# Kernel tuning notes

Hardware: AMD Instinct MI355X
Metric: run time of the kernel (lower is better)

## Reference

```python
import jax, jax.numpy as jnp
import numpy as np
import math

N = 512  # num particles
D = 128  # particle dimension


def setup_inputs() -> dict:
    key = jax.random.key(0)
    particles = jax.random.normal(key, (N, D), dtype=jnp.float32)
    return {"particles": particles}


def reference(particles):
    # particles: [N, D]
    n = particles.shape[0]
    # delta_x[i, j] = particles[j] - particles[i]  (matches unsqueeze(0) - unsqueeze(1))
    delta_x = particles[None, :, :] - particles[:, None, :]   # [N, N, D]
    norm_sq = delta_x * delta_x                               # [N, N, D]

    # mode='univ': per-dimension median over strictly-upper-triangular pairs
    iu_r, iu_c = np.triu_indices(n, k=1)                      # static indices
    sel = norm_sq[iu_r, iu_c, :]                              # [M, D], M = N(N-1)/2
    m = sel.shape[0]
    # torch.median returns the LOWER of the two middle values for even counts
    median = jnp.sort(sel, axis=0)[(m - 1) // 2]              # [D]

    h = median / math.log(n + 1)
    bandwidth = jnp.maximum(h, jnp.asarray(1e-9, dtype=h.dtype))  # [D]

    log_kernel = -(norm_sq / bandwidth)                       # [N, N, D]
    grad_log_kernel = -2.0 * delta_x / bandwidth              # [N, N, D]
    return log_kernel, grad_log_kernel
```

## Files before the change

### kernel.cpp

```cpp
#include <hip/hip_runtime.h>
#include <hip/hip_bf16.h>

#define NP 512
#define DD 128
#define NPAIRS (NP * (NP - 1) / 2)

__device__ __forceinline__ float bitonic512(float r, int tid, float* lds)
{
    for (int k = 2; k <= NP; k <<= 1) {
        for (int s = k >> 1; s > 0; s >>= 1) {
            float other;
            if (s < 64) {
                other = __shfl_xor(r, s);
            } else {
                __syncthreads();
                lds[tid] = r;
                __syncthreads();
                other = lds[tid ^ s];
            }
            const bool lower = (tid & s) == 0;
            const bool up    = (tid & k) == 0;
            r = (lower == up) ? fminf(r, other) : fmaxf(r, other);
        }
    }
    return r;
}

__global__ void __launch_bounds__(512)
median_bw_kernel(const float* __restrict__ particles, float* __restrict__ inv_bw)
{
    const int d = blockIdx.x, tid = threadIdx.x, lane = tid & 63, wid = tid >> 6;

    __shared__ float v[NP];
    __shared__ float cand[NP];
    __shared__ int   cnt_s[2][8];
    __shared__ float sum_s[8];
    __shared__ int   scan_s[8];

    float r = particles[tid * DD + d];
    r = bitonic512(r, tid, v);
    __syncthreads();
    v[tid] = r;
    __syncthreads();

    const float vj = r;
    const int want1 = (NPAIRS - 1) / 2 + 1;

    float s = (tid >= 150) ? (vj - v[tid - 150]) : 0.0f;
    #pragma unroll
    for (int off = 32; off > 0; off >>= 1) s += __shfl_xor(s, off);
    if (lane == 0) sum_s[wid] = s;
    __syncthreads();
    float msum = 0.0f;
    #pragma unroll
    for (int w = 0; w < 8; ++w) msum += sum_s[w];
    const float meanp = fmaxf(msum / 362.0f, 0.0f);

    const float maxd = v[NP - 1] - v[0];
    unsigned lo = 0u;
    unsigned hi = __float_as_uint(maxd) + 1u;
    int C_lo = 0;
    int C_hi = NPAIRS;
    int A = 0, B = tid;
    int buf = 0, round = 0;

    float g_lo = 0.5f - (float)want1;
    float g_hi = (float)(NPAIRS - want1) + 0.5f;
    int   last = 0;

    while (lo < hi) {
        if (C_hi - C_lo <= NP) break;

        const unsigned span = hi - lo;
        unsigned mid;
        if (round == 0) {
            mid = __float_as_uint(meanp);
        } else if ((round & 3) == 3) {
            mid = lo + (span >> 1);
        } else {
            const float flo = __uint_as_float(lo);
            const float fhi = __uint_as_float(hi);
            const float xn  = (flo * g_hi - fhi * g_lo) / (g_hi - g_lo);
            mid = __float_as_uint(xn);
        }
        const unsigned dlt = span >> 3;
        if (mid < lo + dlt)            mid = lo + dlt;
        if (mid > hi - 1u - dlt)       mid = (hi - 1u) - dlt;
        if (mid < lo)                  mid = lo;
        if (mid > hi - 1u)             mid = hi - 1u;
        const float x = __uint_as_float(mid);

        int a = A, b = B;
        while (a < b) {
            const int   m  = (a + b) >> 1;
            const float pv = v[m];
            const bool  t  = (vj - pv <= x);
            b = t ? m : b;
            a = t ? a : m + 1;
        }
        int cnt = tid - a;

        #pragma unroll
        for (int off = 32; off > 0; off >>= 1) cnt += __shfl_xor(cnt, off);
        if (lane == 0) cnt_s[buf][wid] = cnt;
        __syncthreads();
        int tot = 0;
        #pragma unroll
        for (int w = 0; w < 8; ++w) tot += cnt_s[buf][w];

        if (tot >= want1) {
            hi = mid; C_hi = tot; A = a;
            g_hi = (float)(tot - want1) + 0.5f;
            if (last == 1) g_lo *= 0.5f;
            last = 1;
        } else {
            lo = mid + 1u; C_lo = tot; B = a;
            g_lo = (float)(tot - want1) + 0.5f;
            if (last == -1) g_hi *= 0.5f;
            last = -1;
        }
        buf ^= 1;
        ++round;
    }

    if (lo >= hi) {
        if (tid == 0) {
            const float Dk = __uint_as_float(lo);
            const float h  = (Dk * Dk) / 6.240275844172107f;
            inv_bw[d] = 1.0f / fmaxf(h, 1e-9f);
        }
    } else {
        const int T  = C_hi - C_lo;
        const int rr = min(want1 - C_lo, T);
        const int n  = B - A;
        int inc = n;
        #pragma unroll
        for (int off = 1; off < 64; off <<= 1) {
            const int t = __shfl_up(inc, off);
            if (lane >= off) inc += t;
        }
        if (lane == 63) scan_s[wid] = inc;
        __syncthreads();
        int woff = 0;
        #pragma unroll
        for (int w = 0; w < 8; ++w) woff += (w < wid) ? scan_s[w] : 0;
        int off0 = woff + inc - n;
        for (int i = A; i < B; ++i) cand[off0++] = vj - v[i];
        __syncthreads();

        float c = (tid < T) ? cand[tid] : INFINITY;
        c = bitonic512(c, tid, v);

        if (tid == rr - 1) {
            const float Dk = c;
            const float h  = (Dk * Dk) / 6.240275844172107f;
            inv_bw[d] = 1.0f / fmaxf(h, 1e-9f);
        }
    }
}

__global__ void __launch_bounds__(256)
stein_out_kernel(const float* __restrict__ particles,
                 const float* __restrict__ inv_bw,
                 float4* __restrict__ out_lk,
                 float4* __restrict__ out_g)
{
    const float4* __restrict__ p4  = (const float4*)particles;
    const float4* __restrict__ ib4 = (const float4*)inv_bw;
    const int total = NP * NP * (DD / 4);

    for (int t = blockIdx.x * blockDim.x + threadIdx.x; t < total;
         t += gridDim.x * blockDim.x) {
        const int d4 = t & (DD / 4 - 1);
        const int j  = (t >> 5) & (NP - 1);
        const int i  = t >> 14;

        const float4 xj = p4[j * (DD / 4) + d4];
        const float4 xi = p4[i * (DD / 4) + d4];
        const float4 ib = ib4[d4];

        float4 lk, g;
        {
            const float dx = xj.x - xi.x;
            lk.x = -(dx * dx * ib.x);
            g.x  = -2.0f * dx * ib.x;
        }
        {
            const float dx = xj.y - xi.y;
            lk.y = -(dx * dx * ib.y);
            g.y  = -2.0f * dx * ib.y;
        }
        {
            const float dx = xj.z - xi.z;
            lk.z = -(dx * dx * ib.z);
            g.z  = -2.0f * dx * ib.z;
        }
        {
            const float dx = xj.w - xi.w;
            lk.w = -(dx * dx * ib.w);
            g.w  = -2.0f * dx * ib.w;
        }
        out_lk[t] = lk;
        out_g[t]  = g;
    }
}

extern "C" void kernel_launch(void* const* d_in, const int* in_sizes, int n_in,
                              void* d_out, int out_size, void* d_ws, size_t ws_size,
                              hipStream_t stream)
{
    const float* particles = (const float*)d_in[0];
    float* out    = (float*)d_out;
    float* inv_bw = (float*)d_ws;

    median_bw_kernel<<<DD, 512, 0, stream>>>(particles, inv_bw);

    float4* out_lk = (float4*)out;
    float4* out_g  = (float4*)(out + (size_t)NP * NP * DD);
    stein_out_kernel<<<2048, 256, 0, stream>>>(particles, inv_bw, out_lk, out_g);
}
```

Measured before the change: 68.83 us.

## Run median selection search in a single wavefront to drop block barriers

The iterative threshold search for the pairwise-distance median now runs in wavefront 0 only. Each lane handles 8 particles with a fixed-depth, fully unrolled binary search, and the count is reduced with wave shuffles instead of LDS plus a __syncthreads on every round. The per-particle search bounds then go to LDS so the whole block can do the candidate compaction and the final bitonic sort. This removes block-wide barriers from the search loop, at the cost of leaving the other 7 waves idle during it and doing 8 times more serial work per lane.

```diff
diff --git a/kernel.cpp b/kernel.cpp
--- a/kernel.cpp
+++ b/kernel.cpp
@@ -33,9 +33,11 @@
 
     __shared__ float v[NP];
     __shared__ float cand[NP];
-    __shared__ int   cnt_s[2][8];
+    __shared__ int   A_lds[NP];
+    __shared__ int   B_lds[NP];
     __shared__ float sum_s[8];
     __shared__ int   scan_s[8];
+    __shared__ int   done_s, T_s, rr_s;
 
     float r = particles[tid * DD + d];
     r = bitonic512(r, tid, v);
@@ -56,106 +58,155 @@
     for (int w = 0; w < 8; ++w) msum += sum_s[w];
     const float meanp = fmaxf(msum / 362.0f, 0.0f);
 
-    const float maxd = v[NP - 1] - v[0];
-    unsigned lo = 0u;
-    unsigned hi = __float_as_uint(maxd) + 1u;
-    int C_lo = 0;
-    int C_hi = NPAIRS;
-    int A = 0, B = tid;
-    int buf = 0, round = 0;
-
-    float g_lo = 0.5f - (float)want1;
-    float g_hi = (float)(NPAIRS - want1) + 0.5f;
-    int   last = 0;
-
-    while (lo < hi) {
-        if (C_hi - C_lo <= NP) break;
-
-        const unsigned span = hi - lo;
-        unsigned mid;
-        if (round == 0) {
-            mid = __float_as_uint(meanp);
-        } else if ((round & 3) == 3) {
-            mid = lo + (span >> 1);
+    if (wid == 0) {
+        float vjw[8];
+        int   wa[8], wb[8];
+        #pragma unroll
+        for (int w = 0; w < 8; ++w) {
+            const int j = lane + 64 * w;
+            vjw[w] = v[j];
+            wa[w]  = 0;
+            wb[w]  = j;
+        }
+
+        const float maxd = v[NP - 1] - v[0];
+        unsigned lo = 0u;
+        unsigned hi = __float_as_uint(maxd) + 1u;
+        int C_lo = 0, C_hi = NPAIRS;
+        int round = 0, last = 0;
+        float g_lo = 0.5f - (float)want1;
+        float g_hi = (float)(NPAIRS - want1) + 0.5f;
+
+        while (lo < hi) {
+            if (C_hi - C_lo <= NP) break;
+
+            const unsigned span = hi - lo;
+            unsigned mid;
+            if (round == 0) {
+                mid = __float_as_uint(meanp);
+            } else if ((round & 3) == 3) {
+                mid = lo + (span >> 1);
+            } else {
+                const float flo = __uint_as_float(lo);
+                const float fhi = __uint_as_float(hi);
+                const float xn  = (flo * g_hi - fhi * g_lo) / (g_hi - g_lo);
+                mid = __float_as_uint(xn);
+            }
+            const unsigned dlt = span >> 3;
+            if (mid < lo + dlt)      mid = lo + dlt;
+            if (mid > hi - 1u - dlt) mid = (hi - 1u) - dlt;
+            if (mid < lo)            mid = lo;
+            if (mid > hi - 1u)       mid = hi - 1u;
+            const float x = __uint_as_float(mid);
+
+            int a0 = wa[0], b0 = wb[0], a1 = wa[1], b1 = wb[1];
+            int a2 = wa[2], b2 = wb[2], a3 = wa[3], b3 = wb[3];
+            int a4 = wa[4], b4 = wb[4], a5 = wa[5], b5 = wb[5];
+            int a6 = wa[6], b6 = wb[6], a7 = wa[7], b7 = wb[7];
+            #pragma unroll
+            for (int step = 0; step < 9; ++step) {
+                const int m0 = (a0 + b0) >> 1, m1 = (a1 + b1) >> 1;
+                const int m2 = (a2 + b2) >> 1, m3 = (a3 + b3) >> 1;
+                const int m4 = (a4 + b4) >> 1, m5 = (a5 + b5) >> 1;
+                const int m6 = (a6 + b6) >> 1, m7 = (a7 + b7) >> 1;
+                const float p0 = v[m0], p1 = v[m1], p2 = v[m2], p3 = v[m3];
+                const float p4 = v[m4], p5 = v[m5], p6 = v[m6], p7 = v[m7];
+                const bool g0 = a0 < b0, g1 = a1 < b1, g2 = a2 < b2, g3 = a3 < b3;
+                const bool g4 = a4 < b4, g5 = a5 < b5, g6 = a6 < b6, g7 = a7 < b7;
+                const bool t0 = vjw[0] - p0 <= x, t1 = vjw[1] - p1 <= x;
+                const bool t2 = vjw[2] - p2 <= x, t3 = vjw[3] - p3 <= x;
+                const bool t4 = vjw[4] - p4 <= x, t5 = vjw[5] - p5 <= x;
+                const bool t6 = vjw[6] - p6 <= x, t7 = vjw[7] - p7 <= x;
+                b0 = (g0 &  t0) ? m0 : b0;  a0 = (g0 & !t0) ? m0 + 1 : a0;
+                b1 = (g1 &  t1) ? m1 : b1;  a1 = (g1 & !t1) ? m1 + 1 : a1;
+                b2 = (g2 &  t2) ? m2 : b2;  a2 = (g2 & !t2) ? m2 + 1 : a2;
+                b3 = (g3 &  t3) ? m3 : b3;  a3 = (g3 & !t3) ? m3 + 1 : a3;
+                b4 = (g4 &  t4) ? m4 : b4;  a4 = (g4 & !t4) ? m4 + 1 : a4;
+                b5 = (g5 &  t5) ? m5 : b5;  a5 = (g5 & !t5) ? m5 + 1 : a5;
+                b6 = (g6 &  t6) ? m6 : b6;  a6 = (g6 & !t6) ? m6 + 1 : a6;
+                b7 = (g7 &  t7) ? m7 : b7;  a7 = (g7 & !t7) ? m7 + 1 : a7;
+            }
+
+            int cnt = (lane + 0)   - a0;
+            cnt    += (lane + 64)  - a1;
+            cnt    += (lane + 128) - a2;
+            cnt    += (lane + 192) - a3;
+            cnt    += (lane + 256) - a4;
+            cnt    += (lane + 320) - a5;
+            cnt    += (lane + 384) - a6;
+            cnt    += (lane + 448) - a7;
+            #pragma unroll
+            for (int off = 1; off < 64; off <<= 1)
+                cnt += __shfl_xor(cnt, off);
+            const int tot = cnt;
+
+            if (tot >= want1) {
+                hi = mid; C_hi = tot;
+                wa[0]=a0; wa[1]=a1; wa[2]=a2; wa[3]=a3;
+                wa[4]=a4; wa[5]=a5; wa[6]=a6; wa[7]=a7;
+                g_hi = (float)(tot - want1) + 0.5f;
+                if (last == 1) g_lo *= 0.5f;
+                last = 1;
+            } else {
+                lo = mid + 1u; C_lo = tot;
+                wb[0]=a0; wb[1]=a1; wb[2]=a2; wb[3]=a3;
+                wb[4]=a4; wb[5]=a5; wb[6]=a6; wb[7]=a7;
+                g_lo = (float)(tot - want1) + 0.5f;
+                if (last == -1) g_hi *= 0.5f;
+                last = -1;
+            }
+            ++round;
+        }
+
+        if (lo >= hi) {
+            if (lane == 0) {
+                const float Dk = __uint_as_float(lo);
+                const float h  = (Dk * Dk) / 6.240275844172107f;
+                inv_bw[d] = 1.0f / fmaxf(h, 1e-9f);
+                done_s = 1;
+            }
         } else {
-            const float flo = __uint_as_float(lo);
-            const float fhi = __uint_as_float(hi);
-            const float xn  = (flo * g_hi - fhi * g_lo) / (g_hi - g_lo);
-            mid = __float_as_uint(xn);
-        }
-        const unsigned dlt = span >> 3;
-        if (mid < lo + dlt)            mid = lo + dlt;
-        if (mid > hi - 1u - dlt)       mid = (hi - 1u) - dlt;
-        if (mid < lo)                  mid = lo;
-        if (mid > hi - 1u)             mid = hi - 1u;
-        const float x = __uint_as_float(mid);
-
-        int a = A, b = B;
-        while (a < b) {
-            const int   m  = (a + b) >> 1;
-            const float pv = v[m];
-            const bool  t  = (vj - pv <= x);
-            b = t ? m : b;
-            a = t ? a : m + 1;
-        }
-        int cnt = tid - a;
-
-        #pragma unroll
-        for (int off = 32; off > 0; off >>= 1) cnt += __shfl_xor(cnt, off);
-        if (lane == 0) cnt_s[buf][wid] = cnt;
-        __syncthreads();
-        int tot = 0;
-        #pragma unroll
-        for (int w = 0; w < 8; ++w) tot += cnt_s[buf][w];
-
-        if (tot >= want1) {
-            hi = mid; C_hi = tot; A = a;
-            g_hi = (float)(tot - want1) + 0.5f;
-            if (last == 1) g_lo *= 0.5f;
-            last = 1;
-        } else {
-            lo = mid + 1u; C_lo = tot; B = a;
-            g_lo = (float)(tot - want1) + 0.5f;
-            if (last == -1) g_hi *= 0.5f;
-            last = -1;
-        }
-        buf ^= 1;
-        ++round;
-    }
-
-    if (lo >= hi) {
-        if (tid == 0) {
-            const float Dk = __uint_as_float(lo);
-            const float h  = (Dk * Dk) / 6.240275844172107f;
-            inv_bw[d] = 1.0f / fmaxf(h, 1e-9f);
-        }
-    } else {
-        const int T  = C_hi - C_lo;
-        const int rr = min(want1 - C_lo, T);
-        const int n  = B - A;
-        int inc = n;
-        #pragma unroll
-        for (int off = 1; off < 64; off <<= 1) {
-            const int t = __shfl_up(inc, off);
-            if (lane >= off) inc += t;
-        }
-        if (lane == 63) scan_s[wid] = inc;
-        __syncthreads();
-        int woff = 0;
-        #pragma unroll
-        for (int w = 0; w < 8; ++w) woff += (w < wid) ? scan_s[w] : 0;
-        int off0 = woff + inc - n;
-        for (int i = A; i < B; ++i) cand[off0++] = vj - v[i];
-        __syncthreads();
-
-        float c = (tid < T) ? cand[tid] : INFINITY;
-        c = bitonic512(c, tid, v);
-
-        if (tid == rr - 1) {
-            const float Dk = c;
-            const float h  = (Dk * Dk) / 6.240275844172107f;
-            inv_bw[d] = 1.0f / fmaxf(h, 1e-9f);
-        }
+            #pragma unroll
+            for (int w = 0; w < 8; ++w) {
+                A_lds[lane + 64 * w] = wa[w];
+                B_lds[lane + 64 * w] = wb[w];
+            }
+            if (lane == 0) {
+                done_s = 0;
+                T_s    = C_hi - C_lo;
+                rr_s   = min(want1 - C_lo, C_hi - C_lo);
+            }
+        }
+    }
+    __syncthreads();
+    if (done_s) return;
+
+    const int T  = T_s;
+    const int rr = rr_s;
+    const int A  = A_lds[tid], B = B_lds[tid];
+    const int n  = B - A;
+    int inc = n;
+    #pragma unroll
+    for (int off = 1; off < 64; off <<= 1) {
+        const int t = __shfl_up(inc, off);
+        if (lane >= off) inc += t;
+    }
+    if (lane == 63) scan_s[wid] = inc;
+    __syncthreads();
+    int woff = 0;
+    #pragma unroll
+    for (int w = 0; w < 8; ++w) woff += (w < wid) ? scan_s[w] : 0;
+    int off0 = woff + inc - n;
+    for (int i = A; i < B; ++i) cand[off0++] = vj - v[i];
+    __syncthreads();
+
+    float c = (tid < T) ? cand[tid] : INFINITY;
+    c = bitonic512(c, tid, v);
+
+    if (tid == rr - 1) {
+        const float Dk = c;
+        const float h  = (Dk * Dk) / 6.240275844172107f;
+        inv_bw[d] = 1.0f / fmaxf(h, 1e-9f);
     }
 }
 
```

After: 85.22 us. +23.8%, slower.
